# Performance work log

Hardware: AMD Instinct MI355X
Metric: run time of the kernel (lower is better)

## Reference

```python
import jax, jax.numpy as jnp
import numpy as np

N_NODES = 100000
N_EDGES = 1600000
IN_CH = 128
HID_CH = 128   # 2 * out_channels
OUT_CH = 64


def _gcn_conv(x, W, b, src, dst, dinv, n_nodes):
    """PyG GCNConv: x @ W, then sym-normalized scatter-add over edges (self-loops included in src/dst), plus bias."""
    h = x @ W                                   # [N, F_out]
    norm = dinv[src] * dinv[dst]                # [E+N]
    msg = h[src] * norm[:, None]                # [E+N, F_out] -- dominant HBM traffic
    out = jax.ops.segment_sum(msg, dst, num_segments=n_nodes)
    return out + b


def setup_inputs() -> dict:
    key = jax.random.key(0)
    k1, k2, k3, k4 = jax.random.split(key, 4)
    x = jax.random.normal(k1, (N_NODES, IN_CH), dtype=jnp.float32)
    edge_index = jax.random.randint(k2, (2, N_EDGES), 0, N_NODES, dtype=jnp.int64)
    # glorot-ish scaled weights
    W1 = jax.random.normal(k3, (IN_CH, HID_CH), dtype=jnp.float32) * (1.0 / np.sqrt(IN_CH))
    b1 = jnp.zeros((HID_CH,), dtype=jnp.float32)
    W2 = jax.random.normal(k4, (HID_CH, OUT_CH), dtype=jnp.float32) * (1.0 / np.sqrt(HID_CH))
    b2 = jnp.zeros((OUT_CH,), dtype=jnp.float32)
    return {"x": x, "edge_index": edge_index, "W1": W1, "b1": b1, "W2": W2, "b2": b2}


def reference(x, edge_index, W1, b1, W2, b2):
    n = x.shape[0]
    loop = jnp.arange(n, dtype=edge_index.dtype)
    src = jnp.concatenate([edge_index[0], loop])   # add self-loops (GCNConv default)
    dst = jnp.concatenate([edge_index[1], loop])
    # symmetric normalization: deg counted on destination nodes (edge weight = 1)
    deg = jax.ops.segment_sum(jnp.ones_like(dst, dtype=x.dtype), dst, num_segments=n)
    dinv = jnp.where(deg > 0, jax.lax.rsqrt(jnp.maximum(deg, 1.0)), 0.0)
    # conv1 -> ReLU (DFALayer is identity in forward)
    h = jax.nn.relu(_gcn_conv(x, W1, b1, src, dst, dinv, n))
    # conv2 (DFA wrapper is identity in forward)
    return _gcn_conv(h, W2, b2, src, dst, dinv, n)
```

## Files before the change

kernel.cpp:

```cpp
#include <hip/hip_runtime.h>
#include <hip/hip_bf16.h>
#include <cstdint>

typedef short bf16x8 __attribute__((ext_vector_type(8)));
typedef float f32x4 __attribute__((ext_vector_type(4)));
typedef uint uintx4 __attribute__((ext_vector_type(4)));
typedef float floatx4 __attribute__((ext_vector_type(4)));


__device__ inline float blo(uint u) { return __uint_as_float(u << 16); }
__device__ inline float bhi(uint u) { return __uint_as_float(u & 0xffff0000u); }
__device__ inline ushort f2bu(float x) {
    __hip_bfloat16 h = __float2bfloat16(x);
    return *reinterpret_cast<ushort*>(&h);
}
__device__ inline uint fpack2(float x, float y) {
    return (uint)f2bu(x) | ((uint)f2bu(y) << 16);
}

#define ACC8(v, off)                                     \
    acc[(off) + 0] += blo((v).x); acc[(off) + 1] += bhi((v).x); \
    acc[(off) + 2] += blo((v).y); acc[(off) + 3] += bhi((v).y); \
    acc[(off) + 4] += blo((v).z); acc[(off) + 5] += bhi((v).z); \
    acc[(off) + 6] += blo((v).w); acc[(off) + 7] += bhi((v).w);


__global__ __launch_bounds__(256) void hist_k(const int* __restrict__ ei,
                                              uint* __restrict__ hist, int E, int n) {
    __shared__ uint h[256];
    int t = threadIdx.x, blk = blockIdx.x;
    int nb = (n + 511) >> 9;
    h[t] = 0;
    __syncthreads();
    int chunk = (E + 255) / 256;
    int e0 = blk * chunk, e1 = min(E, e0 + chunk);
    for (int e = e0 + t; e < e1; e += 256)
        atomicAdd(&h[((uint)ei[(size_t)E + e]) >> 9], 1u);
    __syncthreads();
    if (t < nb) hist[(size_t)t * 256 + blk] = h[t];
}

__global__ __launch_bounds__(256) void scanA_k(const uint* __restrict__ hist,
                                               uint* __restrict__ histex,
                                               uint* __restrict__ btot) {
    __shared__ uint s[256];
    int t = threadIdx.x, b = blockIdx.x;
    uint v = hist[(size_t)b * 256 + t];
    s[t] = v;
    __syncthreads();
    for (int off = 1; off < 256; off <<= 1) {
        uint u = (t >= off) ? s[t - off] : 0;
        __syncthreads();
        s[t] += u;
        __syncthreads();
    }
    histex[(size_t)b * 256 + t] = s[t] - v;
    if (t == 255) btot[b] = s[255];
}

__global__ __launch_bounds__(256) void scanB_k(const uint* __restrict__ btot,
                                               uint* __restrict__ bbase,
                                               int* __restrict__ rp, int n, int E) {
    __shared__ uint s[256];
    int t = threadIdx.x;
    int nb = (n + 511) >> 9;
    uint v = (t < nb) ? btot[t] : 0;
    s[t] = v;
    __syncthreads();
    for (int off = 1; off < 256; off <<= 1) {
        uint u = (t >= off) ? s[t - off] : 0;
        __syncthreads();
        s[t] += u;
        __syncthreads();
    }
    if (t < nb) bbase[t] = s[t] - v;
    if (t == nb - 1) bbase[nb] = s[t];
    if (t == 0) rp[n] = E;
}

__global__ __launch_bounds__(256) void scat_k(const int* __restrict__ ei,
                                              const uint* __restrict__ bbase,
                                              const uint* __restrict__ histex,
                                              uint* __restrict__ pairs, int E, int n) {
    __shared__ uint cur[256];
    int t = threadIdx.x, blk = blockIdx.x;
    int nb = (n + 511) >> 9;
    if (t < nb) cur[t] = bbase[t] + histex[(size_t)t * 256 + blk];
    __syncthreads();
    int chunk = (E + 255) / 256;
    int e0 = blk * chunk, e1 = min(E, e0 + chunk);
    for (int e = e0 + t; e < e1; e += 256) {
        uint src = (uint)ei[e];
        uint dst = (uint)ei[(size_t)E + e];
        uint p = atomicAdd(&cur[dst >> 9], 1u);
        pairs[p] = (src << 9) | (dst & 511u);
    }
}

__global__ __launch_bounds__(256) void build_k(const uint* __restrict__ pairs,
                                               const uint* __restrict__ bbase,
                                               int* __restrict__ rp,
                                               float* __restrict__ dinv,
                                               int* __restrict__ eb, int n) {
    __shared__ uint lcnt[512];
    __shared__ uint lsc[256];
    int t = threadIdx.x, b = blockIdx.x;
    uint e0 = bbase[b], e1 = bbase[b + 1];
    lcnt[t] = 0;
    lcnt[t + 256] = 0;
    __syncthreads();
    for (uint e = e0 + t; e < e1; e += 256)
        atomicAdd(&lcnt[pairs[e] & 511u], 1u);
    __syncthreads();
    uint c0 = lcnt[2 * t], c1 = lcnt[2 * t + 1];
    uint sm = c0 + c1;
    lsc[t] = sm;
    __syncthreads();
    for (int off = 1; off < 256; off <<= 1) {
        uint u = (t >= off) ? lsc[t - off] : 0;
        __syncthreads();
        lsc[t] += u;
        __syncthreads();
    }
    uint ex = lsc[t] - sm;
    int node0 = (b << 9) + 2 * t;
    if (node0 < n) {
        rp[node0] = (int)(e0 + ex);
        dinv[node0] = rsqrtf((float)(c0 + 1));
    }
    if (node0 + 1 < n) {
        rp[node0 + 1] = (int)(e0 + ex + c0);
        dinv[node0 + 1] = rsqrtf((float)(c1 + 1));
    }
    lcnt[2 * t] = e0 + ex;
    lcnt[2 * t + 1] = e0 + ex + c0;
    __syncthreads();
    for (uint e = e0 + t; e < e1; e += 256) {
        uint p = pairs[e];
        uint pos = atomicAdd(&lcnt[p & 511u], 1u);
        eb[pos] = (int)(p >> 9);
    }
}


__global__ __launch_bounds__(256) void wprep_k(const float* __restrict__ W,
                                               ushort* __restrict__ Wb, int OUTC) {
    int idx = blockIdx.x * 256 + threadIdx.x;
    if (idx >= OUTC * 128) return;
    int k = idx / OUTC, c = idx % OUTC;
    Wb[c * 128 + (k ^ ((c & 7) << 3))] = f2bu(W[idx]);
}


template <int OUTC, bool INB>
__global__ __launch_bounds__(256) void mgemm_k(const void* __restrict__ Xv,
                                               const uint4* __restrict__ Wbv,
                                               const float* __restrict__ dinv,
                                               uint* __restrict__ outb, int n) {
    constexpr int WOFF = 32768;
    constexpr int C4 = OUTC / 4;
    constexpr int NC = OUTC / 16;
    constexpr int LDSB = (32768 + OUTC * 256) > (128 * OUTC * 4)
                             ? (32768 + OUTC * 256) : (128 * OUTC * 4);
    __shared__ uint4 ldsv[LDSB / 16];
    char* lds = (char*)ldsv;

    int t = threadIdx.x;
    int r0b = blockIdx.x * 128;

    for (int i = t; i < OUTC * 16; i += 256)
        ((uint4*)(lds + WOFF))[i] = Wbv[i];

    if constexpr (!INB) {
        for (int i = t; i < 128 * 32; i += 256) {
            int r = i >> 5, kq = i & 31;
            uint2 p = make_uint2(0u, 0u);
            if (r0b + r < n) {
                float di = dinv[r0b + r];
                float4 v = ((const float4*)Xv)[(size_t)(r0b + r) * 32 + kq];
                p = make_uint2(fpack2(v.x * di, v.y * di), fpack2(v.z * di, v.w * di));
            }
            *(uint2*)(lds + r * 256 + ((kq * 8) ^ ((r & 7) << 4))) = p;
        }
    } else {
        for (int i = t; i < 128 * 16; i += 256) {
            int r = i >> 4, kq = i & 15;
            uint4 p = make_uint4(0u, 0u, 0u, 0u);
            if (r0b + r < n)
                p = ((const uint4*)Xv)[((size_t)(kq >> 1) * n + (r0b + r)) * 2 + (kq & 1)];
            *(uint4*)(lds + r * 256 + ((kq * 16) ^ ((r & 7) << 4))) = p;
        }
    }
    __syncthreads();

    int wv = t >> 6, lane = t & 63;
    int l15 = lane & 15, lg = lane >> 4;
    int wr0 = wv * 32;
    int swz = (l15 & 7) << 4;

    f32x4 acc[2][NC];
#pragma unroll
    for (int r = 0; r < 2; ++r)
#pragma unroll
        for (int cj = 0; cj < NC; ++cj) acc[r][cj] = (f32x4){0.f, 0.f, 0.f, 0.f};

#pragma unroll
    for (int kk = 0; kk < 4; ++kk) {
        int koff = kk * 64 + lg * 16;
        bf16x8 a0 = *(bf16x8*)(lds + (wr0 + l15) * 256 + (koff ^ swz));
        bf16x8 a1 = *(bf16x8*)(lds + (wr0 + 16 + l15) * 256 + (koff ^ swz));
#pragma unroll
        for (int cj = 0; cj < NC; ++cj) {
            int c = cj * 16 + l15;
            bf16x8 bv = *(bf16x8*)(lds + WOFF + c * 256 + (koff ^ swz));
            acc[0][cj] = __builtin_amdgcn_mfma_f32_16x16x32_bf16(a0, bv, acc[0][cj], 0, 0, 0);
            acc[1][cj] = __builtin_amdgcn_mfma_f32_16x16x32_bf16(a1, bv, acc[1][cj], 0, 0, 0);
        }
    }
    __syncthreads();

#pragma unroll
    for (int r = 0; r < 2; ++r)
#pragma unroll
        for (int cj = 0; cj < NC; ++cj) {
            int row = wr0 + r * 16 + lg * 4;
            int col = cj * 16 + l15;
#pragma unroll
            for (int j = 0; j < 4; ++j)
                *(float*)(lds + ((size_t)(row + j) * OUTC + col) * 4) = acc[r][cj][j];
        }
    __syncthreads();

    for (int i = t; i < 128 * C4; i += 256) {
        int r = i / C4, c4 = (i % C4) * 4;
        if (r0b + r < n) {
            float4 d = *(float4*)(lds + (size_t)i * 16);
            uint2 p = make_uint2(fpack2(d.x, d.y), fpack2(d.z, d.w));
            ((uint2*)outb)[((size_t)(c4 >> 4) * n + (r0b + r)) * 4 + ((c4 >> 2) & 3)] = p;
        }
    }
}


template <int NPB, int EBCAP>
__global__ __launch_bounds__(128) void agg128v_k(const uint4* __restrict__ hg,
                                                 const int* __restrict__ rp,
                                                 const int* __restrict__ eb,
                                                 const float* __restrict__ dinv,
                                                 const float* __restrict__ bias,
                                                 uint* __restrict__ a1g, int n) {
    __shared__ int ebs[EBCAP];
    int g = blockIdx.x & 7;
    int blkn = blockIdx.x >> 3;
    int t = threadIdx.x;
    const uint4* base = hg + (size_t)g * n * 2;

    int d0 = blkn * NPB;
    int dend = min(n, d0 + NPB);
    int es = rp[d0], ee = rp[dend];
    int cnt = ee - es;
    int scnt = min(cnt, EBCAP);
    for (int i = t; i < scnt; i += 128) ebs[i] = eb[es + i];
    __syncthreads();

    int d = d0 + t;
    bool valid = d < dend;
    int e = 0, e1 = 0;
    float acc[16];
#pragma unroll
    for (int j = 0; j < 16; ++j) acc[j] = 0.f;
    if (valid) {
        e = rp[d] - es;
        e1 = rp[d + 1] - es;
        uint4 s0 = base[(size_t)d * 2];
        uint4 s1 = base[(size_t)d * 2 + 1];
        ACC8(s0, 0);
        ACC8(s1, 8);
    }
    if (cnt <= EBCAP) {
        while (__any(e + 4 <= e1)) {
            if (e + 4 <= e1) {
                int s0 = ebs[e], s1 = ebs[e + 1], s2 = ebs[e + 2], s3 = ebs[e + 3];
                uint4 va0 = base[(size_t)s0 * 2], vb0 = base[(size_t)s0 * 2 + 1];
                uint4 va1 = base[(size_t)s1 * 2], vb1 = base[(size_t)s1 * 2 + 1];
                uint4 va2 = base[(size_t)s2 * 2], vb2 = base[(size_t)s2 * 2 + 1];
                uint4 va3 = base[(size_t)s3 * 2], vb3 = base[(size_t)s3 * 2 + 1];
                ACC8(va0, 0); ACC8(vb0, 8);
                ACC8(va1, 0); ACC8(vb1, 8);
                ACC8(va2, 0); ACC8(vb2, 8);
                ACC8(va3, 0); ACC8(vb3, 8);
                e += 4;
            }
        }
        while (__any(e < e1)) {
            if (e < e1) {
                int s = ebs[e];
                uint4 v0 = base[(size_t)s * 2];
                uint4 v1 = base[(size_t)s * 2 + 1];
                ACC8(v0, 0);
                ACC8(v1, 8);
                ++e;
            }
        }
    } else {
        const int* ebg = eb + es;
        while (__any(e + 4 <= e1)) {
            if (e + 4 <= e1) {
                int s0 = ebg[e], s1 = ebg[e + 1], s2 = ebg[e + 2], s3 = ebg[e + 3];
                uint4 va0 = base[(size_t)s0 * 2], vb0 = base[(size_t)s0 * 2 + 1];
                uint4 va1 = base[(size_t)s1 * 2], vb1 = base[(size_t)s1 * 2 + 1];
                uint4 va2 = base[(size_t)s2 * 2], vb2 = base[(size_t)s2 * 2 + 1];
                uint4 va3 = base[(size_t)s3 * 2], vb3 = base[(size_t)s3 * 2 + 1];
                ACC8(va0, 0); ACC8(vb0, 8);
                ACC8(va1, 0); ACC8(vb1, 8);
                ACC8(va2, 0); ACC8(vb2, 8);
                ACC8(va3, 0); ACC8(vb3, 8);
                e += 4;
            }
        }
        while (__any(e < e1)) {
            if (e < e1) {
                int s = ebg[e];
                uint4 v0 = base[(size_t)s * 2];
                uint4 v1 = base[(size_t)s * 2 + 1];
                ACC8(v0, 0);
                ACC8(v1, 8);
                ++e;
            }
        }
    }
    if (valid) {
        float di = dinv[d];
        const float* bp = bias + g * 16;
        uint o[8];
#pragma unroll
        for (int j = 0; j < 8; ++j)
            o[j] = fpack2(fmaxf(acc[2 * j] * di + bp[2 * j], 0.f) * di,
                          fmaxf(acc[2 * j + 1] * di + bp[2 * j + 1], 0.f) * di);
        uintx4 p0 = {o[0], o[1], o[2], o[3]};
        uintx4 p1 = {o[4], o[5], o[6], o[7]};
        uintx4* dst = (uintx4*)(a1g + ((size_t)g * n + d) * 8);
        __builtin_nontemporal_store(p0, dst);
        __builtin_nontemporal_store(p1, dst + 1);
    }
}

template <int NPB, int EBCAP>
__global__ __launch_bounds__(128) void agg64v_k(const uint4* __restrict__ hg,
                                                const int* __restrict__ rp,
                                                const int* __restrict__ eb,
                                                const float* __restrict__ dinv,
                                                const float* __restrict__ bias,
                                                float* __restrict__ out, int n) {
    __shared__ int ebs[EBCAP];
    int g = blockIdx.x & 3;
    int blkn = blockIdx.x >> 2;
    int t = threadIdx.x;
    const uint4* base = hg + (size_t)g * n * 2;

    int d0 = blkn * NPB;
    int dend = min(n, d0 + NPB);
    int es = rp[d0], ee = rp[dend];
    int cnt = ee - es;
    int scnt = min(cnt, EBCAP);
    for (int i = t; i < scnt; i += 128) ebs[i] = eb[es + i];
    __syncthreads();

    int d = d0 + t;
    bool valid = d < dend;
    int e = 0, e1 = 0;
    float acc[16];
#pragma unroll
    for (int j = 0; j < 16; ++j) acc[j] = 0.f;
    if (valid) {
        e = rp[d] - es;
        e1 = rp[d + 1] - es;
        uint4 s0 = base[(size_t)d * 2];
        uint4 s1 = base[(size_t)d * 2 + 1];
        ACC8(s0, 0);
        ACC8(s1, 8);
    }
    if (cnt <= EBCAP) {
        while (__any(e + 4 <= e1)) {
            if (e + 4 <= e1) {
                int s0 = ebs[e], s1 = ebs[e + 1], s2 = ebs[e + 2], s3 = ebs[e + 3];
                uint4 va0 = base[(size_t)s0 * 2], vb0 = base[(size_t)s0 * 2 + 1];
                uint4 va1 = base[(size_t)s1 * 2], vb1 = base[(size_t)s1 * 2 + 1];
                uint4 va2 = base[(size_t)s2 * 2], vb2 = base[(size_t)s2 * 2 + 1];
                uint4 va3 = base[(size_t)s3 * 2], vb3 = base[(size_t)s3 * 2 + 1];
                ACC8(va0, 0); ACC8(vb0, 8);
                ACC8(va1, 0); ACC8(vb1, 8);
                ACC8(va2, 0); ACC8(vb2, 8);
                ACC8(va3, 0); ACC8(vb3, 8);
                e += 4;
            }
        }
        while (__any(e < e1)) {
            if (e < e1) {
                int s = ebs[e];
                uint4 v0 = base[(size_t)s * 2];
                uint4 v1 = base[(size_t)s * 2 + 1];
                ACC8(v0, 0);
                ACC8(v1, 8);
                ++e;
            }
        }
    } else {
        const int* ebg = eb + es;
        while (__any(e < e1)) {
            if (e < e1) {
                int s = ebg[e];
                uint4 v0 = base[(size_t)s * 2];
                uint4 v1 = base[(size_t)s * 2 + 1];
                ACC8(v0, 0);
                ACC8(v1, 8);
                ++e;
            }
        }
    }
    if (valid) {
        float di = dinv[d];
        const float* bp = bias + g * 16;
        float* op = out + (size_t)d * 64 + g * 16;
#pragma unroll
        for (int q = 0; q < 4; ++q) {
            floatx4 o = {acc[4 * q] * di + bp[4 * q],
                         acc[4 * q + 1] * di + bp[4 * q + 1],
                         acc[4 * q + 2] * di + bp[4 * q + 2],
                         acc[4 * q + 3] * di + bp[4 * q + 3]};
            __builtin_nontemporal_store(o, (floatx4*)(op + 4 * q));
        }
    }
}


extern "C" void kernel_launch(void* const* d_in, const int* in_sizes, int n_in,
                              void* d_out, int out_size, void* d_ws, size_t ws_size,
                              hipStream_t stream) {
    const float* x  = (const float*)d_in[0];
    const int*   ei = (const int*)d_in[1];
    const float* W1 = (const float*)d_in[2];
    const float* b1 = (const float*)d_in[3];
    const float* W2 = (const float*)d_in[4];
    const float* b2 = (const float*)d_in[5];
    float* out = (float*)d_out;

    int n = in_sizes[0] / 128;
    int E = in_sizes[1] / 2;
    int nb = (n + 511) >> 9;

    char* ws = (char*)d_ws;
    size_t o = 0;
    auto alloc = [&](size_t bytes) {
        size_t r = o;
        o = (o + bytes + 255) & ~(size_t)255;
        return r;
    };
    uint*   hist   = (uint*)(ws + alloc((size_t)256 * 256 * 4));
    uint*   histex = (uint*)(ws + alloc((size_t)256 * 256 * 4));
    uint*   btot   = (uint*)(ws + alloc(256 * 4));
    uint*   bbase  = (uint*)(ws + alloc(257 * 4));
    int*    rp     = (int*)(ws + alloc((size_t)(n + 1) * 4));
    float*  dinv   = (float*)(ws + alloc((size_t)n * 4));
    uint*   pairs  = (uint*)(ws + alloc((size_t)E * 4));
    int*    eb     = (int*)(ws + alloc((size_t)E * 4));
    ushort* W1b    = (ushort*)(ws + alloc((size_t)128 * 128 * 2));
    ushort* W2b    = (ushort*)(ws + alloc((size_t)64 * 128 * 2));
    uint*   h1g    = (uint*)(ws + alloc((size_t)n * 64 * 4));
    uint*   a1g    = (uint*)(ws + alloc((size_t)n * 64 * 4));
    uint*   h2g    = (uint*)(ws + alloc((size_t)n * 32 * 4));

    int gB = (n + 127) / 128;
    constexpr int NPB = 128;
    constexpr int EBCAP = 3072;
    int nch = (n + NPB - 1) / NPB;

    hist_k<<<256, 256, 0, stream>>>(ei, hist, E, n);
    scanA_k<<<nb, 256, 0, stream>>>(hist, histex, btot);
    scanB_k<<<1, 256, 0, stream>>>(btot, bbase, rp, n, E);
    scat_k<<<256, 256, 0, stream>>>(ei, bbase, histex, pairs, E, n);
    build_k<<<nb, 256, 0, stream>>>(pairs, bbase, rp, dinv, eb, n);
    wprep_k<<<(128 * 128 + 255) / 256, 256, 0, stream>>>(W1, W1b, 128);
    wprep_k<<<(64 * 128 + 255) / 256, 256, 0, stream>>>(W2, W2b, 64);

    mgemm_k<128, false><<<gB, 256, 0, stream>>>(x, (const uint4*)W1b, dinv, h1g, n);
    agg128v_k<NPB, EBCAP><<<8 * nch, 128, 0, stream>>>((const uint4*)h1g, rp, eb, dinv,
                                                       b1, a1g, n);
    mgemm_k<64, true><<<gB, 256, 0, stream>>>(a1g, (const uint4*)W2b, dinv, h2g, n);
    agg64v_k<NPB, EBCAP><<<4 * nch, 128, 0, stream>>>((const uint4*)h2g, rp, eb, dinv,
                                                      b2, out, n);
}
```

Before: 218.3 us.

## Split each node's 16-feature aggregation across two threads with deeper unroll

Both aggregation kernels now assign two threads per destination node, each gathering one 16-byte half of the 32-byte bf16 feature slice. Nodes per block drop from 128 to 64 so the block size stays at 128 threads, and the edge-buffer capacity is halved to match. The main gather loop is unrolled to 8 edges per iteration. The aim is to double thread-level parallelism and cut per-thread registers so more gathers are in flight. In exchange, each edge index is read by both threads and twice as many blocks load the edge list.

```diff
diff --git a/kernel.cpp b/kernel.cpp
--- a/kernel.cpp
+++ b/kernel.cpp
@@ -18,11 +18,11 @@
     return (uint)f2bu(x) | ((uint)f2bu(y) << 16);
 }
 
-#define ACC8(v, off)                                     \
-    acc[(off) + 0] += blo((v).x); acc[(off) + 1] += bhi((v).x); \
-    acc[(off) + 2] += blo((v).y); acc[(off) + 3] += bhi((v).y); \
-    acc[(off) + 4] += blo((v).z); acc[(off) + 5] += bhi((v).z); \
-    acc[(off) + 6] += blo((v).w); acc[(off) + 7] += bhi((v).w);
+#define ACC8(v)                                          \
+    acc[0] += blo((v).x); acc[1] += bhi((v).x);          \
+    acc[2] += blo((v).y); acc[3] += bhi((v).y);          \
+    acc[4] += blo((v).z); acc[5] += bhi((v).z);          \
+    acc[6] += blo((v).w); acc[7] += bhi((v).w);
 
 
 __global__ __launch_bounds__(256) void hist_k(const int* __restrict__ ei,
@@ -253,7 +253,8 @@
     int g = blockIdx.x & 7;
     int blkn = blockIdx.x >> 3;
     int t = threadIdx.x;
-    const uint4* base = hg + (size_t)g * n * 2;
+    int half = t & 1;
+    const uint4* base = hg + (size_t)g * n * 2 + half;
 
     int d0 = blkn * NPB;
     int dend = min(n, d0 + NPB);
@@ -263,85 +264,81 @@
     for (int i = t; i < scnt; i += 128) ebs[i] = eb[es + i];
     __syncthreads();
 
-    int d = d0 + t;
+    int d = d0 + (t >> 1);
     bool valid = d < dend;
     int e = 0, e1 = 0;
-    float acc[16];
-#pragma unroll
-    for (int j = 0; j < 16; ++j) acc[j] = 0.f;
+    float acc[8];
+#pragma unroll
+    for (int j = 0; j < 8; ++j) acc[j] = 0.f;
     if (valid) {
         e = rp[d] - es;
         e1 = rp[d + 1] - es;
         uint4 s0 = base[(size_t)d * 2];
-        uint4 s1 = base[(size_t)d * 2 + 1];
-        ACC8(s0, 0);
-        ACC8(s1, 8);
+        ACC8(s0);
     }
     if (cnt <= EBCAP) {
-        while (__any(e + 4 <= e1)) {
-            if (e + 4 <= e1) {
+        while (__any(e + 8 <= e1)) {
+            if (e + 8 <= e1) {
                 int s0 = ebs[e], s1 = ebs[e + 1], s2 = ebs[e + 2], s3 = ebs[e + 3];
-                uint4 va0 = base[(size_t)s0 * 2], vb0 = base[(size_t)s0 * 2 + 1];
-                uint4 va1 = base[(size_t)s1 * 2], vb1 = base[(size_t)s1 * 2 + 1];
-                uint4 va2 = base[(size_t)s2 * 2], vb2 = base[(size_t)s2 * 2 + 1];
-                uint4 va3 = base[(size_t)s3 * 2], vb3 = base[(size_t)s3 * 2 + 1];
-                ACC8(va0, 0); ACC8(vb0, 8);
-                ACC8(va1, 0); ACC8(vb1, 8);
-                ACC8(va2, 0); ACC8(vb2, 8);
-                ACC8(va3, 0); ACC8(vb3, 8);
-                e += 4;
+                int s4 = ebs[e + 4], s5 = ebs[e + 5], s6 = ebs[e + 6], s7 = ebs[e + 7];
+                uint4 v0 = base[(size_t)s0 * 2];
+                uint4 v1 = base[(size_t)s1 * 2];
+                uint4 v2 = base[(size_t)s2 * 2];
+                uint4 v3 = base[(size_t)s3 * 2];
+                uint4 v4 = base[(size_t)s4 * 2];
+                uint4 v5 = base[(size_t)s5 * 2];
+                uint4 v6 = base[(size_t)s6 * 2];
+                uint4 v7 = base[(size_t)s7 * 2];
+                ACC8(v0); ACC8(v1); ACC8(v2); ACC8(v3);
+                ACC8(v4); ACC8(v5); ACC8(v6); ACC8(v7);
+                e += 8;
             }
         }
         while (__any(e < e1)) {
             if (e < e1) {
-                int s = ebs[e];
-                uint4 v0 = base[(size_t)s * 2];
-                uint4 v1 = base[(size_t)s * 2 + 1];
-                ACC8(v0, 0);
-                ACC8(v1, 8);
+                uint4 v = base[(size_t)ebs[e] * 2];
+                ACC8(v);
                 ++e;
             }
         }
     } else {
         const int* ebg = eb + es;
-        while (__any(e + 4 <= e1)) {
-            if (e + 4 <= e1) {
+        while (__any(e + 8 <= e1)) {
+            if (e + 8 <= e1) {
                 int s0 = ebg[e], s1 = ebg[e + 1], s2 = ebg[e + 2], s3 = ebg[e + 3];
-                uint4 va0 = base[(size_t)s0 * 2], vb0 = base[(size_t)s0 * 2 + 1];
-                uint4 va1 = base[(size_t)s1 * 2], vb1 = base[(size_t)s1 * 2 + 1];
-                uint4 va2 = base[(size_t)s2 * 2], vb2 = base[(size_t)s2 * 2 + 1];
-                uint4 va3 = base[(size_t)s3 * 2], vb3 = base[(size_t)s3 * 2 + 1];
-                ACC8(va0, 0); ACC8(vb0, 8);
-                ACC8(va1, 0); ACC8(vb1, 8);
-                ACC8(va2, 0); ACC8(vb2, 8);
-                ACC8(va3, 0); ACC8(vb3, 8);
-                e += 4;
+                int s4 = ebg[e + 4], s5 = ebg[e + 5], s6 = ebg[e + 6], s7 = ebg[e + 7];
+                uint4 v0 = base[(size_t)s0 * 2];
+                uint4 v1 = base[(size_t)s1 * 2];
+                uint4 v2 = base[(size_t)s2 * 2];
+                uint4 v3 = base[(size_t)s3 * 2];
+                uint4 v4 = base[(size_t)s4 * 2];
+                uint4 v5 = base[(size_t)s5 * 2];
+                uint4 v6 = base[(size_t)s6 * 2];
+                uint4 v7 = base[(size_t)s7 * 2];
+                ACC8(v0); ACC8(v1); ACC8(v2); ACC8(v3);
+                ACC8(v4); ACC8(v5); ACC8(v6); ACC8(v7);
+                e += 8;
             }
         }
         while (__any(e < e1)) {
             if (e < e1) {
-                int s = ebg[e];
-                uint4 v0 = base[(size_t)s * 2];
-                uint4 v1 = base[(size_t)s * 2 + 1];
-                ACC8(v0, 0);
-                ACC8(v1, 8);
+                uint4 v = base[(size_t)ebg[e] * 2];
+                ACC8(v);
                 ++e;
             }
         }
     }
     if (valid) {
         float di = dinv[d];
-        const float* bp = bias + g * 16;
-        uint o[8];
-#pragma unroll
-        for (int j = 0; j < 8; ++j)
+        const float* bp = bias + g * 16 + half * 8;
+        uint o[4];
+#pragma unroll
+        for (int j = 0; j < 4; ++j)
             o[j] = fpack2(fmaxf(acc[2 * j] * di + bp[2 * j], 0.f) * di,
                           fmaxf(acc[2 * j + 1] * di + bp[2 * j + 1], 0.f) * di);
         uintx4 p0 = {o[0], o[1], o[2], o[3]};
-        uintx4 p1 = {o[4], o[5], o[6], o[7]};
-        uintx4* dst = (uintx4*)(a1g + ((size_t)g * n + d) * 8);
+        uintx4* dst = (uintx4*)(a1g + ((size_t)g * n + d) * 8 + half * 4);
         __builtin_nontemporal_store(p0, dst);
-        __builtin_nontemporal_store(p1, dst + 1);
     }
 }
 
@@ -356,7 +353,8 @@
     int g = blockIdx.x & 3;
     int blkn = blockIdx.x >> 2;
     int t = threadIdx.x;
-    const uint4* base = hg + (size_t)g * n * 2;
+    int half = t & 1;
+    const uint4* base = hg + (size_t)g * n * 2 + half;
 
     int d0 = blkn * NPB;
     int dend = min(n, d0 + NPB);
@@ -366,42 +364,40 @@
     for (int i = t; i < scnt; i += 128) ebs[i] = eb[es + i];
     __syncthreads();
 
-    int d = d0 + t;
+    int d = d0 + (t >> 1);
     bool valid = d < dend;
     int e = 0, e1 = 0;
-    float acc[16];
-#pragma unroll
-    for (int j = 0; j < 16; ++j) acc[j] = 0.f;
+    float acc[8];
+#pragma unroll
+    for (int j = 0; j < 8; ++j) acc[j] = 0.f;
     if (valid) {
         e = rp[d] - es;
         e1 = rp[d + 1] - es;
         uint4 s0 = base[(size_t)d * 2];
-        uint4 s1 = base[(size_t)d * 2 + 1];
-        ACC8(s0, 0);
-        ACC8(s1, 8);
+        ACC8(s0);
     }
     if (cnt <= EBCAP) {
-        while (__any(e + 4 <= e1)) {
-            if (e + 4 <= e1) {
+        while (__any(e + 8 <= e1)) {
+            if (e + 8 <= e1) {
                 int s0 = ebs[e], s1 = ebs[e + 1], s2 = ebs[e + 2], s3 = ebs[e + 3];
-                uint4 va0 = base[(size_t)s0 * 2], vb0 = base[(size_t)s0 * 2 + 1];
-                uint4 va1 = base[(size_t)s1 * 2], vb1 = base[(size_t)s1 * 2 + 1];
-                uint4 va2 = base[(size_t)s2 * 2], vb2 = base[(size_t)s2 * 2 + 1];
-                uint4 va3 = base[(size_t)s3 * 2], vb3 = base[(size_t)s3 * 2 + 1];
-                ACC8(va0, 0); ACC8(vb0, 8);
-                ACC8(va1, 0); ACC8(vb1, 8);
-                ACC8(va2, 0); ACC8(vb2, 8);
-                ACC8(va3, 0); ACC8(vb3, 8);
-                e += 4;
+                int s4 = ebs[e + 4], s5 = ebs[e + 5], s6 = ebs[e + 6], s7 = ebs[e + 7];
+                uint4 v0 = base[(size_t)s0 * 2];
+                uint4 v1 = base[(size_t)s1 * 2];
+                uint4 v2 = base[(size_t)s2 * 2];
+                uint4 v3 = base[(size_t)s3 * 2];
+                uint4 v4 = base[(size_t)s4 * 2];
+                uint4 v5 = base[(size_t)s5 * 2];
+                uint4 v6 = base[(size_t)s6 * 2];
+                uint4 v7 = base[(size_t)s7 * 2];
+                ACC8(v0); ACC8(v1); ACC8(v2); ACC8(v3);
+                ACC8(v4); ACC8(v5); ACC8(v6); ACC8(v7);
+                e += 8;
             }
         }
         while (__any(e < e1)) {
             if (e < e1) {
-                int s = ebs[e];
-                uint4 v0 = base[(size_t)s * 2];
-                uint4 v1 = base[(size_t)s * 2 + 1];
-                ACC8(v0, 0);
-                ACC8(v1, 8);
+                uint4 v = base[(size_t)ebs[e] * 2];
+                ACC8(v);
                 ++e;
             }
         }
@@ -409,27 +405,22 @@
         const int* ebg = eb + es;
         while (__any(e < e1)) {
             if (e < e1) {
-                int s = ebg[e];
-                uint4 v0 = base[(size_t)s * 2];
-                uint4 v1 = base[(size_t)s * 2 + 1];
-                ACC8(v0, 0);
-                ACC8(v1, 8);
+                uint4 v = base[(size_t)ebg[e] * 2];
+                ACC8(v);
                 ++e;
             }
         }
     }
     if (valid) {
         float di = dinv[d];
-        const float* bp = bias + g * 16;
-        float* op = out + (size_t)d * 64 + g * 16;
-#pragma unroll
-        for (int q = 0; q < 4; ++q) {
-            floatx4 o = {acc[4 * q] * di + bp[4 * q],
-                         acc[4 * q + 1] * di + bp[4 * q + 1],
-                         acc[4 * q + 2] * di + bp[4 * q + 2],
-                         acc[4 * q + 3] * di + bp[4 * q + 3]};
-            __builtin_nontemporal_store(o, (floatx4*)(op + 4 * q));
-        }
+        const float* bp = bias + g * 16 + half * 8;
+        float* op = out + (size_t)d * 64 + g * 16 + half * 8;
+        floatx4 o0 = {acc[0] * di + bp[0], acc[1] * di + bp[1],
+                      acc[2] * di + bp[2], acc[3] * di + bp[3]};
+        floatx4 o1 = {acc[4] * di + bp[4], acc[5] * di + bp[5],
+                      acc[6] * di + bp[6], acc[7] * di + bp[7]};
+        __builtin_nontemporal_store(o0, (floatx4*)op);
+        __builtin_nontemporal_store(o1, (floatx4*)(op + 4));
     }
 }
 
@@ -471,8 +462,8 @@
     uint*   h2g    = (uint*)(ws + alloc((size_t)n * 32 * 4));
 
     int gB = (n + 127) / 128;
-    constexpr int NPB = 128;
-    constexpr int EBCAP = 3072;
+    constexpr int NPB = 64;
+    constexpr int EBCAP = 1536;
     int nch = (n + NPB - 1) / NPB;
 
     hist_k<<<256, 256, 0, stream>>>(ei, hist, E, n);
```

After: 209.9 us. 3.9% less time.
